# Kernel optimization log

Measured on AMD Instinct MI355X. Metric: run time of the kernel, lower is better.

## Reference

```python
import jax, jax.numpy as jnp
import numpy as np

H = 4          # heads (both HGTConv and MHA)
LN_EPS = 1e-5
ALPHA = 0.1


def _ln(x, g, b):
    m = x.mean(-1, keepdims=True)
    v = ((x - m) ** 2).mean(-1, keepdims=True)
    return (x - m) * jax.lax.rsqrt(v + LN_EPS) * g + b


def _kqv(x, Wk, bk, Wq, bq, Wv, bv, D):
    N = x.shape[0]
    k = (x @ Wk.T + bk).reshape(N, H, D)
    q = (x @ Wq.T + bq).reshape(N, H, D)
    v = (x @ Wv.T + bv).reshape(N, H, D)
    return k, q, v


def _hgt_edge(q_dst, k_src, v_src, a_rel, m_rel, p_rel, src, dst, n_dst):
    """PyG HGTConv message passing for one edge type: relation-transform,
    per-dst-node softmax, weighted scatter-sum."""
    D = q_dst.shape[-1]
    k = jnp.einsum('nhd,hde->nhe', k_src, a_rel)   # [N_src,H,D]
    v = jnp.einsum('nhd,hde->nhe', v_src, m_rel)
    logit = (q_dst[dst] * k[src]).sum(-1) * p_rel / np.sqrt(D)   # [E,H]
    mx = jax.ops.segment_max(logit, dst, num_segments=n_dst)
    e = jnp.exp(logit - mx[dst])
    s = jax.ops.segment_sum(e, dst, num_segments=n_dst)
    a = e / (s[dst] + 1e-16)
    return jax.ops.segment_sum(v[src] * a[..., None], dst, num_segments=n_dst)  # [N_dst,H,D]


def _hgt_out(agg, x, Wout, bout, skip):
    N, dim = x.shape
    o = jax.nn.gelu(agg.reshape(N, dim), approximate=False) @ Wout.T + bout
    a = jax.nn.sigmoid(skip)
    return a * o + (1.0 - a) * x


def _mha(x, Wi, bi, Wo, bo):
    # self-attention over all entities as a single sequence (batch=1)
    N, dim = x.shape
    D = dim // H
    q, k, v = jnp.split(x @ Wi.T + bi, 3, axis=-1)
    q = q.reshape(N, H, D).transpose(1, 0, 2)
    k = k.reshape(N, H, D).transpose(1, 0, 2)
    v = v.reshape(N, H, D).transpose(1, 0, 2)
    att = jax.nn.softmax(jnp.einsum('hnd,hmd->hnm', q, k) / np.sqrt(D), axis=-1)
    o = jnp.einsum('hnm,hmd->hnd', att, v).transpose(1, 0, 2).reshape(N, dim)
    return o @ Wo.T + bo


def _forward(x_entity, x_passage, query_emb,
             Wk_ent, bk_ent, Wq_ent, bq_ent, Wv_ent, bv_ent, Wout_ent, bout_ent, skip_ent,
             Wk_psg, bk_psg, Wq_psg, bq_psg, Wv_psg, bv_psg, Wout_psg, bout_psg, skip_psg,
             a_e2p, m_e2p, p_e2p, a_p2e, m_p2e, p_p2e,
             mha_in_w, mha_in_b, mha_out_w, mha_out_b,
             ln_ent_g, ln_ent_b, ln_psg_g, ln_psg_b,
             w1, b1, w2, b2,
             e2p_src, e2p_dst, p2e_src, p2e_dst):
    N_e, dim = x_entity.shape
    N_p = x_passage.shape[0]
    D = dim // H
    # ---- HGTConv ----
    k_e, q_e, v_e = _kqv(x_entity, Wk_ent, bk_ent, Wq_ent, bq_ent, Wv_ent, bv_ent, D)
    k_p, q_p, v_p = _kqv(x_passage, Wk_psg, bk_psg, Wq_psg, bq_psg, Wv_psg, bv_psg, D)
    agg_p = _hgt_edge(q_p, k_e, v_e, a_e2p, m_e2p, p_e2p, e2p_src, e2p_dst, N_p)
    agg_e = _hgt_edge(q_e, k_p, v_p, a_p2e, m_p2e, p_p2e, p2e_src, p2e_dst, N_e)
    h_ent = _hgt_out(agg_e, x_entity, Wout_ent, bout_ent, skip_ent)
    h_psg = _hgt_out(agg_p, x_passage, Wout_psg, bout_psg, skip_psg)
    # ---- global entity attention + residual mix + LN ----
    h_glob = _mha(h_ent, mha_in_w, mha_in_b, mha_out_w, mha_out_b)
    h_ent = _ln((1.0 - ALPHA) * h_ent + ALPHA * h_glob, ln_ent_g, ln_ent_b)
    # ---- gather-scale-scatter entity -> passage (kernel target) ----
    q = query_emb.reshape(-1)
    rel = jax.nn.sigmoid(h_ent @ q)                          # [N_e]
    w_ent = h_ent[e2p_src] * rel[e2p_src][:, None]           # gather + scale
    ctx = jax.ops.segment_sum(w_ent, e2p_dst, num_segments=N_p)  # scatter-add
    h_psg = _ln(h_psg + ctx, ln_psg_g, ln_psg_b)
    # ---- scoring head ----
    feats = jnp.concatenate([h_psg, jnp.broadcast_to(q, (N_p, dim))], axis=-1)
    scores = (jax.nn.relu(feats @ w1.T + b1) @ w2.T + b2).squeeze(-1)
    return scores


def setup_inputs() -> dict:
    key = jax.random.key(0)
    N_E, N_P, DIM, NE = 4096, 4096, 256, 262144
    D = DIM // H
    ks = iter(jax.random.split(key, 64))
    def rn(shape, s=1.0):
        return jax.random.normal(next(ks), shape, jnp.float32) * s
    w = 0.05
    inp = {
        'x_entity': rn((N_E, DIM)),
        'x_passage': rn((N_P, DIM)),
        'query_emb': rn((DIM,)),
    }
    for t in ('ent', 'psg'):
        inp['Wk_' + t] = rn((DIM, DIM), w); inp['bk_' + t] = jnp.zeros((DIM,))
        inp['Wq_' + t] = rn((DIM, DIM), w); inp['bq_' + t] = jnp.zeros((DIM,))
        inp['Wv_' + t] = rn((DIM, DIM), w); inp['bv_' + t] = jnp.zeros((DIM,))
        inp['Wout_' + t] = rn((DIM, DIM), w); inp['bout_' + t] = jnp.zeros((DIM,))
        inp['skip_' + t] = jnp.ones(())
    for e in ('e2p', 'p2e'):
        inp['a_' + e] = rn((H, D, D), w)
        inp['m_' + e] = rn((H, D, D), w)
        inp['p_' + e] = jnp.ones((H,))
    inp['mha_in_w'] = rn((3 * DIM, DIM), w); inp['mha_in_b'] = jnp.zeros((3 * DIM,))
    inp['mha_out_w'] = rn((DIM, DIM), w); inp['mha_out_b'] = jnp.zeros((DIM,))
    inp['ln_ent_g'] = jnp.ones((DIM,)); inp['ln_ent_b'] = jnp.zeros((DIM,))
    inp['ln_psg_g'] = jnp.ones((DIM,)); inp['ln_psg_b'] = jnp.zeros((DIM,))
    inp['w1'] = rn((DIM, 2 * DIM), w); inp['b1'] = jnp.zeros((DIM,))
    inp['w2'] = rn((1, DIM), w); inp['b2'] = jnp.zeros((1,))
    inp['e2p_src'] = jax.random.randint(next(ks), (NE,), 0, N_E, jnp.int32)
    inp['e2p_dst'] = jax.random.randint(next(ks), (NE,), 0, N_P, jnp.int32)
    inp['p2e_src'] = jax.random.randint(next(ks), (NE,), 0, N_P, jnp.int32)
    inp['p2e_dst'] = jax.random.randint(next(ks), (NE,), 0, N_E, jnp.int32)
    return inp


def reference(x_entity, x_passage, query_emb,
              Wk_ent, bk_ent, Wq_ent, bq_ent, Wv_ent, bv_ent, Wout_ent, bout_ent, skip_ent,
              Wk_psg, bk_psg, Wq_psg, bq_psg, Wv_psg, bv_psg, Wout_psg, bout_psg, skip_psg,
              a_e2p, m_e2p, p_e2p, a_p2e, m_p2e, p_p2e,
              mha_in_w, mha_in_b, mha_out_w, mha_out_b,
              ln_ent_g, ln_ent_b, ln_psg_g, ln_psg_b,
              w1, b1, w2, b2,
              e2p_src, e2p_dst, p2e_src, p2e_dst):
    return _forward(x_entity, x_passage, query_emb,
                    Wk_ent, bk_ent, Wq_ent, bq_ent, Wv_ent, bv_ent, Wout_ent, bout_ent, skip_ent,
                    Wk_psg, bk_psg, Wq_psg, bq_psg, Wv_psg, bv_psg, Wout_psg, bout_psg, skip_psg,
                    a_e2p, m_e2p, p_e2p, a_p2e, m_p2e, p_p2e,
                    mha_in_w, mha_in_b, mha_out_w, mha_out_b,
                    ln_ent_g, ln_ent_b, ln_psg_g, ln_psg_b,
                    w1, b1, w2, b2,
                    e2p_src, e2p_dst, p2e_src, p2e_dst)
```

## Files before the change

### kernel.cpp

```cpp
#include <hip/hip_runtime.h>
#include <hip/hip_bf16.h>
#include <math.h>

#define DIM 256
#define NHEAD 4
#define HD 64
#define MSPLIT 4

typedef __attribute__((ext_vector_type(8))) short short8b;
typedef __attribute__((ext_vector_type(4))) float f32x4;

union B8 { uint4 u; short8b v; };

__device__ __forceinline__ float sigmoidf_(float x) { return 1.0f / (1.0f + __expf(-x)); }
__device__ __forceinline__ float geluf_(float x) {
    return 0.5f * x * (1.0f + erff(x * 0.70710678118654752440f));
}
__device__ __forceinline__ float wave_sum64(float v) {
    v += __shfl_xor(v, 32); v += __shfl_xor(v, 16); v += __shfl_xor(v, 8);
    v += __shfl_xor(v, 4);  v += __shfl_xor(v, 2);  v += __shfl_xor(v, 1);
    return v;
}
__device__ __forceinline__ unsigned short f2bf(float f) {
    union { float f; unsigned int u; } a; a.f = f;
    unsigned int u = a.u;
    unsigned int r = (u + 0x7FFFu + ((u >> 16) & 1u)) >> 16;
    return (unsigned short)r;
}
__device__ __forceinline__ unsigned int pk2bf(float lo, float hi) {
    return (unsigned int)f2bf(lo) | ((unsigned int)f2bf(hi) << 16);
}

template<int DO_GELU>
__launch_bounds__(256)
__global__ void cvt_bf16_kernel(const float* __restrict__ src,
                                unsigned short* __restrict__ dst, int n8)
{
    const int i = blockIdx.x * 256 + threadIdx.x;
    if (i >= n8) return;
    float4 a = reinterpret_cast<const float4*>(src)[2 * i];
    float4 b = reinterpret_cast<const float4*>(src)[2 * i + 1];
    if (DO_GELU) {
        a.x = geluf_(a.x); a.y = geluf_(a.y); a.z = geluf_(a.z); a.w = geluf_(a.w);
        b.x = geluf_(b.x); b.y = geluf_(b.y); b.z = geluf_(b.z); b.w = geluf_(b.w);
    }
    ushort4 lo = {f2bf(a.x), f2bf(a.y), f2bf(a.z), f2bf(a.w)};
    ushort4 hi = {f2bf(b.x), f2bf(b.y), f2bf(b.z), f2bf(b.w)};
    reinterpret_cast<ushort4*>(dst)[2 * i] = lo;
    reinterpret_cast<ushort4*>(dst)[2 * i + 1] = hi;
}

__launch_bounds__(256)
__global__ void cvt_w_kernel(const float* __restrict__ W0, const float* __restrict__ W1,
                             const float* __restrict__ W2, const float* __restrict__ W3,
                             const float* __restrict__ W4, const float* __restrict__ W5,
                             const float* __restrict__ W6, const float* __restrict__ W7,
                             const float* __restrict__ W8, const float* __restrict__ W9,
                             const float* __restrict__ W10, const float* __restrict__ W11,
                             unsigned short* __restrict__ arena)
{
    const float* s;
    switch (blockIdx.y) {
        case 0: s = W0; break;  case 1: s = W1; break;  case 2: s = W2; break;
        case 3: s = W3; break;  case 4: s = W4; break;  case 5: s = W5; break;
        case 6: s = W6; break;  case 7: s = W7; break;  case 8: s = W8; break;
        case 9: s = W9; break;  case 10: s = W10; break; default: s = W11; break;
    }
    const int i = blockIdx.x * 256 + threadIdx.x;
    unsigned short* dst = arena + (size_t)blockIdx.y * 65536;
    float4 a = reinterpret_cast<const float4*>(s)[2 * i];
    float4 b = reinterpret_cast<const float4*>(s)[2 * i + 1];
    ushort4 lo = {f2bf(a.x), f2bf(a.y), f2bf(a.z), f2bf(a.w)};
    ushort4 hi = {f2bf(b.x), f2bf(b.y), f2bf(b.z), f2bf(b.w)};
    reinterpret_cast<ushort4*>(dst)[2 * i] = lo;
    reinterpret_cast<ushort4*>(dst)[2 * i + 1] = hi;
}

template<int OUT_MODE, int WF32, int WBF>
__launch_bounds__(256)
__global__ void bgemm_kernel(const unsigned short* __restrict__ Abf,
                             const unsigned short* __restrict__ W0b,
                             const unsigned short* __restrict__ W1b,
                             const unsigned short* __restrict__ W2b,
                             const float* __restrict__ B0, const float* __restrict__ B1,
                             const float* __restrict__ B2,
                             float* __restrict__ C, int ldc,
                             unsigned short* __restrict__ Cbf, int ldcb,
                             const float* __restrict__ xres,
                             const float* __restrict__ skipv)
{
    const int t = threadIdx.x;
    const int lane = t & 63;
    const int wid = t >> 6;
    const int col16 = lane & 15;
    const int oct = lane >> 4;
    const int r0 = blockIdx.y * 64 + wid * 16;
    const int c0 = blockIdx.x * 64;
    const int widx = c0 >> 8;
    const unsigned short* W = (widx == 0) ? W0b : (widx == 1 ? W1b : W2b);
    const float* Bv = (widx == 0) ? B0 : (widx == 1 ? B1 : B2);
    const int cw = c0 & 255;

    const unsigned short* aptr = Abf + (size_t)(r0 + col16) * 256 + oct * 8;
    const unsigned short* wptr = W + (size_t)(cw + col16) * 256 + oct * 8;

    f32x4 acc0 = {0,0,0,0}, acc1 = {0,0,0,0}, acc2 = {0,0,0,0}, acc3 = {0,0,0,0};
#pragma unroll
    for (int k0 = 0; k0 < 256; k0 += 32) {
        B8 af, w0, w1, w2, w3;
        af.u = *reinterpret_cast<const uint4*>(aptr + k0);
        w0.u = *reinterpret_cast<const uint4*>(wptr + k0);
        w1.u = *reinterpret_cast<const uint4*>(wptr + k0 + 16 * 256);
        w2.u = *reinterpret_cast<const uint4*>(wptr + k0 + 32 * 256);
        w3.u = *reinterpret_cast<const uint4*>(wptr + k0 + 48 * 256);
        acc0 = __builtin_amdgcn_mfma_f32_16x16x32_bf16(af.v, w0.v, acc0, 0, 0, 0);
        acc1 = __builtin_amdgcn_mfma_f32_16x16x32_bf16(af.v, w1.v, acc1, 0, 0, 0);
        acc2 = __builtin_amdgcn_mfma_f32_16x16x32_bf16(af.v, w2.v, acc2, 0, 0, 0);
        acc3 = __builtin_amdgcn_mfma_f32_16x16x32_bf16(af.v, w3.v, acc3, 0, 0, 0);
    }

    float bias[4];
#pragma unroll
    for (int j = 0; j < 4; ++j) bias[j] = Bv[cw + j * 16 + col16];
    float sg = 0.f;
    if (OUT_MODE == 1) sg = sigmoidf_(skipv[0]);

    const float av[4][4] = {
        {acc0.x, acc0.y, acc0.z, acc0.w}, {acc1.x, acc1.y, acc1.z, acc1.w},
        {acc2.x, acc2.y, acc2.z, acc2.w}, {acc3.x, acc3.y, acc3.z, acc3.w}};
#pragma unroll
    for (int r = 0; r < 4; ++r) {
        const int row = r0 + oct * 4 + r;
#pragma unroll
        for (int j = 0; j < 4; ++j) {
            const int col = c0 + j * 16 + col16;
            float v = av[j][r] + bias[j];
            if (OUT_MODE == 1) {
                const float xv = xres[(size_t)row * ldc + col];
                v = sg * v + (1.f - sg) * xv;
            }
            if (WF32) C[(size_t)row * ldc + col] = v;
            if (WBF)  Cbf[(size_t)row * ldcb + col] = f2bf(v);
        }
    }
}

template<int IN_GELU, int OUT_MODE>
__launch_bounds__(256)
__global__ void gemm_kernel(const float* __restrict__ A, int lda,
                            const float* __restrict__ W0, const float* __restrict__ W1,
                            const float* __restrict__ W2, int ldw,
                            const float* __restrict__ B0, const float* __restrict__ B1,
                            const float* __restrict__ B2,
                            float* __restrict__ C, int ldc, int Kin,
                            float* __restrict__ scores,
                            const float* __restrict__ w2v,
                            const float* __restrict__ b2v)
{
    __shared__ float As[16][68];
    __shared__ float Ws[16][68];
    const int t = threadIdx.x;
    const int r0 = blockIdx.y * 64;
    const int c0 = blockIdx.x * 64;
    const int widx = c0 >> 8;
    const float* W  = (widx == 0) ? W0 : (widx == 1 ? W1 : W2);
    const float* Bv = (widx == 0) ? B0 : (widx == 1 ? B1 : B2);
    const int cw = c0 & 255;

    const int lrow = t >> 2;
    const int lk   = (t & 3) << 2;
    const int ty = t >> 4, tx = t & 15;

    const float* Aptr = A + (size_t)(r0 + lrow) * lda + lk;
    const float* Wptr = W + (size_t)(cw + lrow) * ldw + lk;

    float acc[4][4] = {};
    for (int k0 = 0; k0 < Kin; k0 += 16) {
        float4 av = *reinterpret_cast<const float4*>(Aptr + k0);
        float4 wv = *reinterpret_cast<const float4*>(Wptr + k0);
        if (IN_GELU) {
            av.x = geluf_(av.x); av.y = geluf_(av.y);
            av.z = geluf_(av.z); av.w = geluf_(av.w);
        }
        As[lk + 0][lrow] = av.x; As[lk + 1][lrow] = av.y;
        As[lk + 2][lrow] = av.z; As[lk + 3][lrow] = av.w;
        Ws[lk + 0][lrow] = wv.x; Ws[lk + 1][lrow] = wv.y;
        Ws[lk + 2][lrow] = wv.z; Ws[lk + 3][lrow] = wv.w;
        __syncthreads();
#pragma unroll
        for (int k = 0; k < 16; ++k) {
            const float4 a = *reinterpret_cast<const float4*>(&As[k][ty << 2]);
            const float4 b = *reinterpret_cast<const float4*>(&Ws[k][tx << 2]);
            const float ar[4] = {a.x, a.y, a.z, a.w};
            const float br[4] = {b.x, b.y, b.z, b.w};
#pragma unroll
            for (int i = 0; i < 4; ++i)
#pragma unroll
                for (int j = 0; j < 4; ++j)
                    acc[i][j] = fmaf(ar[i], br[j], acc[i][j]);
        }
        __syncthreads();
    }

    float bias[4];
#pragma unroll
    for (int j = 0; j < 4; ++j) bias[j] = Bv[cw + (tx << 2) + j];

    if (OUT_MODE == 0) {
#pragma unroll
        for (int i = 0; i < 4; ++i) {
            float4 st;
            st.x = acc[i][0] + bias[0]; st.y = acc[i][1] + bias[1];
            st.z = acc[i][2] + bias[2]; st.w = acc[i][3] + bias[3];
            *reinterpret_cast<float4*>(&C[(size_t)(r0 + (ty << 2) + i) * ldc + c0 + (tx << 2)]) = st;
        }
    } else {
        float wv[4];
#pragma unroll
        for (int j = 0; j < 4; ++j) wv[j] = w2v[c0 + (tx << 2) + j];
#pragma unroll
        for (int i = 0; i < 4; ++i) {
            float p = 0.f;
#pragma unroll
            for (int j = 0; j < 4; ++j)
                p = fmaf(fmaxf(acc[i][j] + bias[j], 0.f), wv[j], p);
            if (c0 == 0 && tx == 0) p += b2v[0];
            atomicAdd(&scores[r0 + (ty << 2) + i], p);
        }
    }
}

__launch_bounds__(256)
__global__ void rel_transform_kernel(const float* __restrict__ kin, int ldin,
                                     const float* __restrict__ arel,
                                     float* __restrict__ kout)
{
    __shared__ float Al[64][68];
    __shared__ float Kl[64][65];
    const int t = threadIdx.x;
    const int r0 = blockIdx.x * 64;
    const int h = blockIdx.y;
    const float* ah = arel + h * 4096;
    for (int i = t; i < 1024; i += 256) {
        const int rr = i >> 4, c4 = (i & 15) << 2;
        const float4 av = *reinterpret_cast<const float4*>(&ah[rr * 64 + c4]);
        *reinterpret_cast<float4*>(&Al[rr][c4]) = av;
        const float4 kv = *reinterpret_cast<const float4*>(&kin[(size_t)(r0 + rr) * ldin + h * 64 + c4]);
        Kl[rr][c4 + 0] = kv.x; Kl[rr][c4 + 1] = kv.y;
        Kl[rr][c4 + 2] = kv.z; Kl[rr][c4 + 3] = kv.w;
    }
    __syncthreads();
    const int r  = t & 63;
    const int e0 = (t >> 6) << 4;
    float acc[16] = {};
    for (int d = 0; d < 64; ++d) {
        const float kv = Kl[r][d];
#pragma unroll
        for (int u4 = 0; u4 < 4; ++u4) {
            const float4 a = *reinterpret_cast<const float4*>(&Al[d][e0 + (u4 << 2)]);
            acc[u4 * 4 + 0] = fmaf(kv, a.x, acc[u4 * 4 + 0]);
            acc[u4 * 4 + 1] = fmaf(kv, a.y, acc[u4 * 4 + 1]);
            acc[u4 * 4 + 2] = fmaf(kv, a.z, acc[u4 * 4 + 2]);
            acc[u4 * 4 + 3] = fmaf(kv, a.w, acc[u4 * 4 + 3]);
        }
    }
#pragma unroll
    for (int u4 = 0; u4 < 4; ++u4) {
        float4 st = {acc[u4 * 4 + 0], acc[u4 * 4 + 1], acc[u4 * 4 + 2], acc[u4 * 4 + 3]};
        *reinterpret_cast<float4*>(&kout[(size_t)(r0 + r) * 256 + h * 64 + e0 + (u4 << 2)]) = st;
    }
}

__global__ void edge_count_kernel(const int* __restrict__ dst, int* __restrict__ cnt, int E)
{
    const int i = blockIdx.x * 256 + threadIdx.x;
    if (i < E) atomicAdd(&cnt[dst[i]], 1);
}

__launch_bounds__(1024)
__global__ void scan_kernel(const int* __restrict__ cnt, int* __restrict__ indptr,
                            int* __restrict__ cursor)
{
    __shared__ int sh[1024];
    const int t = threadIdx.x;
    const int4 v = *reinterpret_cast<const int4*>(&cnt[t << 2]);
    const int sum = v.x + v.y + v.z + v.w;
    sh[t] = sum;
    __syncthreads();
    for (int off = 1; off < 1024; off <<= 1) {
        int x = 0;
        if (t >= off) x = sh[t - off];
        __syncthreads();
        if (t >= off) sh[t] += x;
        __syncthreads();
    }
    int run = sh[t] - sum;
    const int base = t << 2;
    if (t == 0) indptr[0] = 0;
    cursor[base + 0] = run; run += v.x; indptr[base + 1] = run;
    cursor[base + 1] = run; run += v.y; indptr[base + 2] = run;
    cursor[base + 2] = run; run += v.z; indptr[base + 3] = run;
    cursor[base + 3] = run; run += v.w; indptr[base + 4] = run;
}

__global__ void edge_scatter_kernel(const int* __restrict__ src, const int* __restrict__ dst,
                                    int* __restrict__ cursor, int* __restrict__ ssrc, int E)
{
    const int i = blockIdx.x * 256 + threadIdx.x;
    if (i < E) {
        const int p = atomicAdd(&cursor[dst[i]], 1);
        ssrc[p] = src[i];
    }
}

__launch_bounds__(256)
__global__ void hgt_attn_kernel(const float* __restrict__ qdst,
                                const float* __restrict__ kt,
                                const float* __restrict__ vt,
                                const float* __restrict__ prel,
                                const int* __restrict__ indptr,
                                const int* __restrict__ ssrc,
                                float* __restrict__ agg)
{
    const int n = blockIdx.x * 4 + (threadIdx.x >> 6);
    const int lane = threadIdx.x & 63;
    const int h = lane >> 4;
    const int d4 = (lane & 15) << 2;
    const float4 q = *reinterpret_cast<const float4*>(&qdst[(size_t)n * 768 + h * 64 + d4]);
    const float ps = prel[h] * 0.125f;
    const int e0 = indptr[n], e1 = indptr[n + 1];
    float m = -1e30f, s = 0.f;
    float4 acc = {0.f, 0.f, 0.f, 0.f};
    for (int e = e0; e < e1; ++e) {
        const int sr = ssrc[e];
        const float4 k = *reinterpret_cast<const float4*>(&kt[(size_t)sr * 256 + h * 64 + d4]);
        float d = q.x * k.x + q.y * k.y + q.z * k.z + q.w * k.w;
        d += __shfl_xor(d, 1); d += __shfl_xor(d, 2);
        d += __shfl_xor(d, 4); d += __shfl_xor(d, 8);
        const float logit = d * ps;
        const float mn = fmaxf(m, logit);
        const float f = __expf(m - mn);
        const float p = __expf(logit - mn);
        s = s * f + p;
        const float4 v = *reinterpret_cast<const float4*>(&vt[(size_t)sr * 256 + h * 64 + d4]);
        acc.x = acc.x * f + p * v.x;
        acc.y = acc.y * f + p * v.y;
        acc.z = acc.z * f + p * v.z;
        acc.w = acc.w * f + p * v.w;
        m = mn;
    }
    const float inv = 1.f / (s + 1e-16f);
    float4 st = {acc.x * inv, acc.y * inv, acc.z * inv, acc.w * inv};
    *reinterpret_cast<float4*>(&agg[(size_t)n * 256 + h * 64 + d4]) = st;
}

__launch_bounds__(256)
__global__ void vtrans_kernel(const unsigned short* __restrict__ qkv_bf,
                              unsigned short* __restrict__ vt, int N)
{
    __shared__ unsigned short tile[64][66];
    const int t = threadIdx.x;
    const int k0 = blockIdx.x * 64;
    const int h = blockIdx.y;
    {
        const int key = t >> 2;
        const int d0 = (t & 3) << 4;
        const unsigned short* src = qkv_bf + (size_t)(k0 + key) * 768 + 512 + h * 64 + d0;
        const uint4 a = *reinterpret_cast<const uint4*>(src);
        const uint4 b = *reinterpret_cast<const uint4*>(src + 8);
        const unsigned int w_[8] = {a.x, a.y, a.z, a.w, b.x, b.y, b.z, b.w};
#pragma unroll
        for (int j = 0; j < 8; ++j) {
            tile[d0 + 2 * j][key]     = (unsigned short)(w_[j] & 0xffff);
            tile[d0 + 2 * j + 1][key] = (unsigned short)(w_[j] >> 16);
        }
    }
    __syncthreads();
    {
        const int d = t >> 2;
        const int kk = (t & 3) << 4;
        unsigned int o_[8];
#pragma unroll
        for (int j = 0; j < 8; ++j)
            o_[j] = (unsigned int)tile[d][kk + 2 * j] | ((unsigned int)tile[d][kk + 2 * j + 1] << 16);
        unsigned short* dstp = vt + (size_t)(h * 64 + d) * N + k0 + kk;
        uint4 s0 = {o_[0], o_[1], o_[2], o_[3]};
        uint4 s1 = {o_[4], o_[5], o_[6], o_[7]};
        *reinterpret_cast<uint4*>(dstp) = s0;
        *reinterpret_cast<uint4*>(dstp + 8) = s1;
    }
}

__launch_bounds__(256)
__global__ void mha_mfma_kernel(const unsigned short* __restrict__ qkv_bf,
                                const unsigned short* __restrict__ vt_bf,
                                float* __restrict__ opart,
                                float* __restrict__ mpart,
                                float* __restrict__ lpart,
                                int N)
{
    const int lane = threadIdx.x & 63;
    const int g = lane >> 4;
    const int q15 = lane & 15;
    const int gw = blockIdx.x * 4 + (threadIdx.x >> 6);
    const int split = gw & (MSPLIT - 1);
    const int gq = gw >> 2;
    const int h = gq >> 8;
    const int qt = gq & 255;
    const int q0 = qt * 16;
    const int kbeg = split * (N / MSPLIT);
    const int kend = kbeg + (N / MSPLIT);

    B8 qf0, qf1;
    {
        const unsigned short* qp = qkv_bf + (size_t)(q0 + q15) * 768 + h * 64 + g * 8;
        qf0.u = *reinterpret_cast<const uint4*>(qp);
        qf1.u = *reinterpret_cast<const uint4*>(qp + 32);
    }

    f32x4 o0 = {0,0,0,0}, o1 = {0,0,0,0}, o2 = {0,0,0,0}, o3 = {0,0,0,0};
    float m_run = -1e30f, l_run = 0.f;

    const unsigned short* kbase = qkv_bf + 256 + h * 64 + g * 8;
    const unsigned short* vbase = vt_bf + (size_t)(h * 64 + q15) * N + g * 8;
    const int sl0 = (((2 * g) & 3) << 4) + q15;
    const int sl1 = (((2 * g + 1) & 3) << 4) + q15;

    for (int ck = kbeg; ck < kend; ck += 32) {
        B8 k00, k01, k10, k11;
        const unsigned short* kp0 = kbase + (size_t)(ck + q15) * 768;
        const unsigned short* kp1 = kbase + (size_t)(ck + 16 + q15) * 768;
        k00.u = *reinterpret_cast<const uint4*>(kp0);
        k01.u = *reinterpret_cast<const uint4*>(kp0 + 32);
        k10.u = *reinterpret_cast<const uint4*>(kp1);
        k11.u = *reinterpret_cast<const uint4*>(kp1 + 32);
        f32x4 s0 = {0,0,0,0}, s1 = {0,0,0,0};
        s0 = __builtin_amdgcn_mfma_f32_16x16x32_bf16(k00.v, qf0.v, s0, 0, 0, 0);
        s0 = __builtin_amdgcn_mfma_f32_16x16x32_bf16(k01.v, qf1.v, s0, 0, 0, 0);
        s1 = __builtin_amdgcn_mfma_f32_16x16x32_bf16(k10.v, qf0.v, s1, 0, 0, 0);
        s1 = __builtin_amdgcn_mfma_f32_16x16x32_bf16(k11.v, qf1.v, s1, 0, 0, 0);

        float p[8];
        p[0] = s0.x * 0.125f; p[1] = s0.y * 0.125f; p[2] = s0.z * 0.125f; p[3] = s0.w * 0.125f;
        p[4] = s1.x * 0.125f; p[5] = s1.y * 0.125f; p[6] = s1.z * 0.125f; p[7] = s1.w * 0.125f;

        float mx = fmaxf(fmaxf(fmaxf(p[0], p[1]), fmaxf(p[2], p[3])),
                         fmaxf(fmaxf(p[4], p[5]), fmaxf(p[6], p[7])));
        mx = fmaxf(mx, __shfl_xor(mx, 16));
        mx = fmaxf(mx, __shfl_xor(mx, 32));
        const float mnew = fmaxf(m_run, mx);
        const float f = __expf(m_run - mnew);
        float sum = 0.f;
#pragma unroll
        for (int i = 0; i < 8; ++i) { p[i] = __expf(p[i] - mnew); sum += p[i]; }
        sum += __shfl_xor(sum, 16);
        sum += __shfl_xor(sum, 32);
        l_run = l_run * f + sum;
        m_run = mnew;
        o0 *= f; o1 *= f; o2 *= f; o3 *= f;

        const unsigned int c01a = pk2bf(p[0], p[1]), c23a = pk2bf(p[2], p[3]);
        const unsigned int c01b = pk2bf(p[4], p[5]), c23b = pk2bf(p[6], p[7]);
        uint4 pu;
        {
            unsigned int x0, x1;
            x0 = (unsigned int)__shfl((int)c01a, sl0); x1 = (unsigned int)__shfl((int)c01b, sl0);
            pu.x = (g < 2) ? x0 : x1;
            x0 = (unsigned int)__shfl((int)c23a, sl0); x1 = (unsigned int)__shfl((int)c23b, sl0);
            pu.y = (g < 2) ? x0 : x1;
            x0 = (unsigned int)__shfl((int)c01a, sl1); x1 = (unsigned int)__shfl((int)c01b, sl1);
            pu.z = (g < 2) ? x0 : x1;
            x0 = (unsigned int)__shfl((int)c23a, sl1); x1 = (unsigned int)__shfl((int)c23b, sl1);
            pu.w = (g < 2) ? x0 : x1;
        }
        B8 pb; pb.u = pu;

        const unsigned short* vp = vbase + ck;
        B8 vf;
        vf.u = *reinterpret_cast<const uint4*>(vp);
        o0 = __builtin_amdgcn_mfma_f32_16x16x32_bf16(vf.v, pb.v, o0, 0, 0, 0);
        vf.u = *reinterpret_cast<const uint4*>(vp + (size_t)16 * N);
        o1 = __builtin_amdgcn_mfma_f32_16x16x32_bf16(vf.v, pb.v, o1, 0, 0, 0);
        vf.u = *reinterpret_cast<const uint4*>(vp + (size_t)32 * N);
        o2 = __builtin_amdgcn_mfma_f32_16x16x32_bf16(vf.v, pb.v, o2, 0, 0, 0);
        vf.u = *reinterpret_cast<const uint4*>(vp + (size_t)48 * N);
        o3 = __builtin_amdgcn_mfma_f32_16x16x32_bf16(vf.v, pb.v, o3, 0, 0, 0);
    }

    float* op = opart + (size_t)split * N * 256 + (size_t)(q0 + q15) * 256 + h * 64 + 4 * g;
#pragma unroll
    for (int r = 0; r < 4; ++r) {
        op[0 * 16 + r] = o0[r];
        op[1 * 16 + r] = o1[r];
        op[2 * 16 + r] = o2[r];
        op[3 * 16 + r] = o3[r];
    }
    if (g == 0) {
        mpart[(size_t)(split * NHEAD + h) * N + q0 + q15] = m_run;
        lpart[(size_t)(split * NHEAD + h) * N + q0 + q15] = l_run;
    }
}

__launch_bounds__(256)
__global__ void mha_combine_kernel(const float* __restrict__ opart,
                                   const float* __restrict__ mpart,
                                   const float* __restrict__ lpart,
                                   unsigned short* __restrict__ outpb, int N)
{
    const int q = blockIdx.x;
    const int c = threadIdx.x;
    const int h = c >> 6;
    const size_t base = (size_t)q * 256 + c;
    float m[MSPLIT], l[MSPLIT];
    float M = -1e30f;
#pragma unroll
    for (int s = 0; s < MSPLIT; ++s) {
        m[s] = mpart[(size_t)(s * NHEAD + h) * N + q];
        l[s] = lpart[(size_t)(s * NHEAD + h) * N + q];
        M = fmaxf(M, m[s]);
    }
    float L = 0.f, o = 0.f;
#pragma unroll
    for (int s = 0; s < MSPLIT; ++s) {
        const float w = __expf(m[s] - M);
        L += w * l[s];
        o = fmaf(w, opart[(size_t)s * N * 256 + base], o);
    }
    outpb[base] = f2bf(o / L);
}

__launch_bounds__(256)
__global__ void mix_ln_rel_kernel(float* __restrict__ he, const float* __restrict__ hg,
                                  const float* __restrict__ g, const float* __restrict__ b,
                                  const float* __restrict__ q, float* __restrict__ rel)
{
    const int row = (blockIdx.x * 256 + threadIdx.x) >> 6;
    const int lane = threadIdx.x & 63;
    const float4 a = *reinterpret_cast<const float4*>(&he[(size_t)row * 256 + (lane << 2)]);
    const float4 c = *reinterpret_cast<const float4*>(&hg[(size_t)row * 256 + (lane << 2)]);
    float4 v;
    v.x = 0.9f * a.x + 0.1f * c.x; v.y = 0.9f * a.y + 0.1f * c.y;
    v.z = 0.9f * a.z + 0.1f * c.z; v.w = 0.9f * a.w + 0.1f * c.w;
    const float mean = wave_sum64(v.x + v.y + v.z + v.w) * (1.f / 256.f);
    float4 d = {v.x - mean, v.y - mean, v.z - mean, v.w - mean};
    const float var = wave_sum64(d.x * d.x + d.y * d.y + d.z * d.z + d.w * d.w) * (1.f / 256.f);
    const float rs = rsqrtf(var + 1e-5f);
    const float4 gg = *reinterpret_cast<const float4*>(&g[lane << 2]);
    const float4 bb = *reinterpret_cast<const float4*>(&b[lane << 2]);
    float4 y = {d.x * rs * gg.x + bb.x, d.y * rs * gg.y + bb.y,
                d.z * rs * gg.z + bb.z, d.w * rs * gg.w + bb.w};
    *reinterpret_cast<float4*>(&he[(size_t)row * 256 + (lane << 2)]) = y;
    const float4 qq = *reinterpret_cast<const float4*>(&q[lane << 2]);
    const float dq = wave_sum64(y.x * qq.x + y.y * qq.y + y.z * qq.z + y.w * qq.w);
    if (lane == 0) rel[row] = sigmoidf_(dq);
}

__launch_bounds__(256)
__global__ void ctx_gather_kernel(const float* __restrict__ he, const float* __restrict__ rel,
                                  const int* __restrict__ indptr, const int* __restrict__ ssrc,
                                  float* __restrict__ ctx)
{
    const int gw = (blockIdx.x * 256 + threadIdx.x) >> 6;
    const int lane = threadIdx.x & 63;
    const int p = gw >> 2, qt = gw & 3;
    const int e0 = indptr[p], e1 = indptr[p + 1];
    float acc = 0.f;
    for (int e = e0; e < e1; ++e) {
        const int sr = ssrc[e];
        acc = fmaf(he[(size_t)sr * 256 + qt * 64 + lane], rel[sr], acc);
    }
    ctx[(size_t)p * 256 + qt * 64 + lane] = acc;
}

__launch_bounds__(256)
__global__ void psg_ln_kernel(float* __restrict__ hp, const float* __restrict__ ctx,
                              const float* __restrict__ g, const float* __restrict__ b)
{
    const int row = (blockIdx.x * 256 + threadIdx.x) >> 6;
    const int lane = threadIdx.x & 63;
    const float4 a = *reinterpret_cast<const float4*>(&hp[(size_t)row * 256 + (lane << 2)]);
    const float4 c = *reinterpret_cast<const float4*>(&ctx[(size_t)row * 256 + (lane << 2)]);
    float4 v = {a.x + c.x, a.y + c.y, a.z + c.z, a.w + c.w};
    const float mean = wave_sum64(v.x + v.y + v.z + v.w) * (1.f / 256.f);
    float4 d = {v.x - mean, v.y - mean, v.z - mean, v.w - mean};
    const float var = wave_sum64(d.x * d.x + d.y * d.y + d.z * d.z + d.w * d.w) * (1.f / 256.f);
    const float rs = rsqrtf(var + 1e-5f);
    const float4 gg = *reinterpret_cast<const float4*>(&g[lane << 2]);
    const float4 bb = *reinterpret_cast<const float4*>(&b[lane << 2]);
    float4 y = {d.x * rs * gg.x + bb.x, d.y * rs * gg.y + bb.y,
                d.z * rs * gg.z + bb.z, d.w * rs * gg.w + bb.w};
    *reinterpret_cast<float4*>(&hp[(size_t)row * 256 + (lane << 2)]) = y;
}

__global__ void qterm_kernel(const float* __restrict__ w1, const float* __restrict__ b1,
                             const float* __restrict__ q, float* __restrict__ qterm)
{
    __shared__ float qs[256];
    const int t = threadIdx.x;
    qs[t] = q[t];
    __syncthreads();
    float s = b1[t];
    for (int k = 0; k < 256; ++k) s = fmaf(w1[(size_t)t * 512 + 256 + k], qs[k], s);
    qterm[t] = s;
}

extern "C" void kernel_launch(void* const* d_in, const int* in_sizes, int n_in,
                              void* d_out, int out_size, void* d_ws, size_t ws_size,
                              hipStream_t stream)
{
    const float* x_ent = (const float*)d_in[0];
    const float* x_psg = (const float*)d_in[1];
    const float* q_emb = (const float*)d_in[2];
    const float* Wk_e = (const float*)d_in[3];  const float* bk_e = (const float*)d_in[4];
    const float* Wq_e = (const float*)d_in[5];  const float* bq_e = (const float*)d_in[6];
    const float* Wv_e = (const float*)d_in[7];  const float* bv_e = (const float*)d_in[8];
    const float* Wo_e = (const float*)d_in[9];  const float* bo_e = (const float*)d_in[10];
    const float* sk_e = (const float*)d_in[11];
    const float* Wk_p = (const float*)d_in[12]; const float* bk_p = (const float*)d_in[13];
    const float* Wq_p = (const float*)d_in[14]; const float* bq_p = (const float*)d_in[15];
    const float* Wv_p = (const float*)d_in[16]; const float* bv_p = (const float*)d_in[17];
    const float* Wo_p = (const float*)d_in[18]; const float* bo_p = (const float*)d_in[19];
    const float* sk_p = (const float*)d_in[20];
    const float* a_e2p = (const float*)d_in[21];
    const float* m_e2p = (const float*)d_in[22];
    const float* p_e2p = (const float*)d_in[23];
    const float* a_p2e = (const float*)d_in[24];
    const float* m_p2e = (const float*)d_in[25];
    const float* p_p2e = (const float*)d_in[26];
    const float* Wmi = (const float*)d_in[27];  const float* bmi = (const float*)d_in[28];
    const float* Wmo = (const float*)d_in[29];  const float* bmo = (const float*)d_in[30];
    const float* lng_e = (const float*)d_in[31]; const float* lnb_e = (const float*)d_in[32];
    const float* lng_p = (const float*)d_in[33]; const float* lnb_p = (const float*)d_in[34];
    const float* w1 = (const float*)d_in[35];   const float* b1 = (const float*)d_in[36];
    const float* w2 = (const float*)d_in[37];   const float* b2 = (const float*)d_in[38];
    const int* e2p_src = (const int*)d_in[39];
    const int* e2p_dst = (const int*)d_in[40];
    const int* p2e_src = (const int*)d_in[41];
    const int* p2e_dst = (const int*)d_in[42];

    const int NE = in_sizes[0] / DIM;
    const int NP = in_sizes[1] / DIM;
    const int E  = in_sizes[39];
    float* scores = (float*)d_out;

    char* wp = (char*)d_ws;
    auto alloc = [&](size_t bytes) -> void* {
        void* r = (void*)wp;
        wp += (bytes + 255) & ~(size_t)255;
        return r;
    };
    float* kqv_e = (float*)alloc((size_t)NE * 768 * 4);
    float* kqv_p = (float*)alloc((size_t)NP * 768 * 4);
    float* kt_e  = (float*)alloc((size_t)NE * 256 * 4);
    float* vt_e  = (float*)alloc((size_t)NE * 256 * 4);
    float* kt_p  = (float*)alloc((size_t)NP * 256 * 4);
    float* vt_p  = (float*)alloc((size_t)NP * 256 * 4);
    float* agg_p = (float*)alloc((size_t)NP * 256 * 4);
    float* agg_e = (float*)alloc((size_t)NE * 256 * 4);
    float* h_ent = (float*)alloc((size_t)NE * 256 * 4);
    float* h_psg = (float*)alloc((size_t)NP * 256 * 4);
    float* h_glob= (float*)alloc((size_t)NE * 256 * 4);
    float* relv  = (float*)alloc((size_t)NE * 4);
    float* ctxb  = (float*)alloc((size_t)NP * 256 * 4);
    float* qterm = (float*)alloc(256 * 4);
    unsigned short* warena  = (unsigned short*)alloc((size_t)12 * 65536 * 2);
    unsigned short* xe_bf   = (unsigned short*)alloc((size_t)NE * 256 * 2);
    unsigned short* xp_bf   = (unsigned short*)alloc((size_t)NP * 256 * 2);
    unsigned short* ge_bf   = (unsigned short*)alloc((size_t)NE * 256 * 2);
    unsigned short* gp_bf   = (unsigned short*)alloc((size_t)NP * 256 * 2);
    unsigned short* hent_bf = (unsigned short*)alloc((size_t)NE * 256 * 2);
    unsigned short* atto_bf = (unsigned short*)alloc((size_t)NE * 256 * 2);
    unsigned short* qkv_bf  = (unsigned short*)alloc((size_t)NE * 768 * 2);
    unsigned short* vt_bf   = (unsigned short*)alloc((size_t)256 * NE * 2);
    float* mpart = (float*)alloc((size_t)MSPLIT * NHEAD * NE * 4);
    float* lpart = (float*)alloc((size_t)MSPLIT * NHEAD * NE * 4);
    float* opart = kqv_e;
    int* cnt_a = (int*)alloc((size_t)NP * 4);
    int* cur_a = (int*)alloc((size_t)NP * 4);
    int* ip_a  = (int*)alloc((size_t)(NP + 1) * 4);
    int* ss_a  = (int*)alloc((size_t)E * 4);
    int* cnt_b = (int*)alloc((size_t)NE * 4);
    int* cur_b = (int*)alloc((size_t)NE * 4);
    int* ip_b  = (int*)alloc((size_t)(NE + 1) * 4);
    int* ss_b  = (int*)alloc((size_t)E * 4);

    hipMemsetAsync(cnt_a, 0, (size_t)NP * 4, stream);
    hipMemsetAsync(cnt_b, 0, (size_t)NE * 4, stream);
    hipMemsetAsync(d_out, 0, (size_t)out_size * 4, stream);

    cvt_w_kernel<<<dim3(32, 12), 256, 0, stream>>>(
        Wk_e, Wq_e, Wv_e, Wo_e, Wk_p, Wq_p, Wv_p, Wo_p,
        Wmi, Wmi + 65536, Wmi + 131072, Wmo, warena);
    cvt_bf16_kernel<0><<<NE * 256 / 2048, 256, 0, stream>>>(x_ent, xe_bf, NE * 32);
    cvt_bf16_kernel<0><<<NP * 256 / 2048, 256, 0, stream>>>(x_psg, xp_bf, NP * 32);

    const int eb = (E + 255) / 256;
    edge_count_kernel<<<eb, 256, 0, stream>>>(e2p_dst, cnt_a, E);
    edge_count_kernel<<<eb, 256, 0, stream>>>(p2e_dst, cnt_b, E);
    scan_kernel<<<1, 1024, 0, stream>>>(cnt_a, ip_a, cur_a);
    scan_kernel<<<1, 1024, 0, stream>>>(cnt_b, ip_b, cur_b);
    edge_scatter_kernel<<<eb, 256, 0, stream>>>(e2p_src, e2p_dst, cur_a, ss_a, E);
    edge_scatter_kernel<<<eb, 256, 0, stream>>>(p2e_src, p2e_dst, cur_b, ss_b, E);

    bgemm_kernel<0,1,0><<<dim3(12, NE / 64), 256, 0, stream>>>(
        xe_bf, warena, warena + 65536, warena + 131072, bk_e, bq_e, bv_e,
        kqv_e, 768, nullptr, 0, nullptr, nullptr);
    bgemm_kernel<0,1,0><<<dim3(12, NP / 64), 256, 0, stream>>>(
        xp_bf, warena + 4*65536, warena + 5*65536, warena + 6*65536, bk_p, bq_p, bv_p,
        kqv_p, 768, nullptr, 0, nullptr, nullptr);

    rel_transform_kernel<<<dim3(NE / 64, NHEAD), 256, 0, stream>>>(kqv_e + 0,   768, a_e2p, kt_e);
    rel_transform_kernel<<<dim3(NE / 64, NHEAD), 256, 0, stream>>>(kqv_e + 512, 768, m_e2p, vt_e);
    rel_transform_kernel<<<dim3(NP / 64, NHEAD), 256, 0, stream>>>(kqv_p + 0,   768, a_p2e, kt_p);
    rel_transform_kernel<<<dim3(NP / 64, NHEAD), 256, 0, stream>>>(kqv_p + 512, 768, m_p2e, vt_p);

    hgt_attn_kernel<<<NP / 4, 256, 0, stream>>>(kqv_p + 256, kt_e, vt_e, p_e2p, ip_a, ss_a, agg_p);
    hgt_attn_kernel<<<NE / 4, 256, 0, stream>>>(kqv_e + 256, kt_p, vt_p, p_p2e, ip_b, ss_b, agg_e);

    cvt_bf16_kernel<1><<<NE * 256 / 2048, 256, 0, stream>>>(agg_e, ge_bf, NE * 32);
    cvt_bf16_kernel<1><<<NP * 256 / 2048, 256, 0, stream>>>(agg_p, gp_bf, NP * 32);
    bgemm_kernel<1,1,1><<<dim3(4, NE / 64), 256, 0, stream>>>(
        ge_bf, warena + 3*65536, warena + 3*65536, warena + 3*65536, bo_e, bo_e, bo_e,
        h_ent, 256, hent_bf, 256, x_ent, sk_e);
    bgemm_kernel<1,1,0><<<dim3(4, NP / 64), 256, 0, stream>>>(
        gp_bf, warena + 7*65536, warena + 7*65536, warena + 7*65536, bo_p, bo_p, bo_p,
        h_psg, 256, nullptr, 0, x_psg, sk_p);

    bgemm_kernel<0,0,1><<<dim3(12, NE / 64), 256, 0, stream>>>(
        hent_bf, warena + 8*65536, warena + 9*65536, warena + 10*65536,
        bmi, bmi + 256, bmi + 512,
        nullptr, 0, qkv_bf, 768, nullptr, nullptr);
    vtrans_kernel<<<dim3(NE / 64, NHEAD), 256, 0, stream>>>(qkv_bf, vt_bf, NE);
    mha_mfma_kernel<<<NHEAD * (NE / 16) * MSPLIT / 4, 256, 0, stream>>>(
        qkv_bf, vt_bf, opart, mpart, lpart, NE);
    mha_combine_kernel<<<NE, 256, 0, stream>>>(opart, mpart, lpart, atto_bf, NE);
    bgemm_kernel<0,1,0><<<dim3(4, NE / 64), 256, 0, stream>>>(
        atto_bf, warena + 11*65536, warena + 11*65536, warena + 11*65536, bmo, bmo, bmo,
        h_glob, 256, nullptr, 0, nullptr, nullptr);

    mix_ln_rel_kernel<<<NE / 4, 256, 0, stream>>>(h_ent, h_glob, lng_e, lnb_e, q_emb, relv);

    ctx_gather_kernel<<<NP, 256, 0, stream>>>(h_ent, relv, ip_a, ss_a, ctxb);
    psg_ln_kernel<<<NP / 4, 256, 0, stream>>>(h_psg, ctxb, lng_p, lnb_p);

    qterm_kernel<<<1, 256, 0, stream>>>(w1, b1, q_emb, qterm);
    gemm_kernel<0,2><<<dim3(4, NP / 64), 256, 0, stream>>>(
        h_psg, 256, w1, w1, w1, 512, qterm, qterm, qterm,
        nullptr, 256, 256, scores, w2, b2);
}
```

Measured before the change: 717.2 us.

## Rewrite MHA kernel with 32x32 MFMA tiles, permlane swaps, and prefetch HGT gathers

The flash-attention style MHA kernel now uses 32x32x16 bf16 MFMA on 32-query tiles instead of 16x16x32 on 16-query tiles. It builds the P operand with the hardware packed bf16 convert and permlane32 swaps rather than many shuffles, and doubles the key split count to keep enough waves in flight. The HGT edge attention loop also software-prefetches the next edge's K/V rows. This aims to cut cross-lane shuffle overhead and memory latency stalls, at the cost of higher register pressure and larger partial buffers for the combine step.

```diff
diff --git a/kernel.cpp b/kernel.cpp
--- a/kernel.cpp
+++ b/kernel.cpp
@@ -5,10 +5,12 @@
 #define DIM 256
 #define NHEAD 4
 #define HD 64
-#define MSPLIT 4
+#define MSPLIT 8
 
 typedef __attribute__((ext_vector_type(8))) short short8b;
 typedef __attribute__((ext_vector_type(4))) float f32x4;
+typedef __attribute__((ext_vector_type(16))) float f32x16;
+typedef __attribute__((ext_vector_type(2))) unsigned int uint2v;
 
 union B8 { uint4 u; short8b v; };
 
@@ -27,8 +29,13 @@
     unsigned int r = (u + 0x7FFFu + ((u >> 16) & 1u)) >> 16;
     return (unsigned short)r;
 }
-__device__ __forceinline__ unsigned int pk2bf(float lo, float hi) {
-    return (unsigned int)f2bf(lo) | ((unsigned int)f2bf(hi) << 16);
+__device__ __forceinline__ unsigned int cvtpk_(float lo, float hi) {
+    unsigned int r;
+    asm("v_cvt_pk_bf16_f32 %0, %1, %2" : "=v"(r) : "v"(lo), "v"(hi));
+    return r;
+}
+__device__ __forceinline__ uint2v plswap_(unsigned int a, unsigned int b) {
+    return __builtin_amdgcn_permlane32_swap(a, b, false, false);
 }
 
 template<int DO_GELU>
@@ -331,9 +338,17 @@
     const int e0 = indptr[n], e1 = indptr[n + 1];
     float m = -1e30f, s = 0.f;
     float4 acc = {0.f, 0.f, 0.f, 0.f};
+    float4 kc = {0.f, 0.f, 0.f, 0.f}, vc = {0.f, 0.f, 0.f, 0.f};
+    if (e0 < e1) {
+        const int sr0 = ssrc[e0];
+        kc = *reinterpret_cast<const float4*>(&kt[(size_t)sr0 * 256 + h * 64 + d4]);
+        vc = *reinterpret_cast<const float4*>(&vt[(size_t)sr0 * 256 + h * 64 + d4]);
+    }
     for (int e = e0; e < e1; ++e) {
-        const int sr = ssrc[e];
-        const float4 k = *reinterpret_cast<const float4*>(&kt[(size_t)sr * 256 + h * 64 + d4]);
+        const float4 k = kc, v = vc;
+        const int nsr = ssrc[(e + 1 < e1) ? (e + 1) : e];
+        kc = *reinterpret_cast<const float4*>(&kt[(size_t)nsr * 256 + h * 64 + d4]);
+        vc = *reinterpret_cast<const float4*>(&vt[(size_t)nsr * 256 + h * 64 + d4]);
         float d = q.x * k.x + q.y * k.y + q.z * k.z + q.w * k.w;
         d += __shfl_xor(d, 1); d += __shfl_xor(d, 2);
         d += __shfl_xor(d, 4); d += __shfl_xor(d, 8);
@@ -342,7 +357,6 @@
         const float f = __expf(m - mn);
         const float p = __expf(logit - mn);
         s = s * f + p;
-        const float4 v = *reinterpret_cast<const float4*>(&vt[(size_t)sr * 256 + h * 64 + d4]);
         acc.x = acc.x * f + p * v.x;
         acc.y = acc.y * f + p * v.y;
         acc.z = acc.z * f + p * v.z;
@@ -400,104 +414,113 @@
                                 int N)
 {
     const int lane = threadIdx.x & 63;
-    const int g = lane >> 4;
-    const int q15 = lane & 15;
+    const int l31 = lane & 31;
+    const int hi = lane >> 5;
     const int gw = blockIdx.x * 4 + (threadIdx.x >> 6);
     const int split = gw & (MSPLIT - 1);
-    const int gq = gw >> 2;
-    const int h = gq >> 8;
-    const int qt = gq & 255;
-    const int q0 = qt * 16;
+    const int gq = gw / MSPLIT;
+    const int h = gq >> 7;
+    const int qt = gq & 127;
+    const int q0 = qt * 32;
     const int kbeg = split * (N / MSPLIT);
     const int kend = kbeg + (N / MSPLIT);
 
-    B8 qf0, qf1;
+    B8 qf0, qf1, qf2, qf3;
     {
-        const unsigned short* qp = qkv_bf + (size_t)(q0 + q15) * 768 + h * 64 + g * 8;
+        const unsigned short* qp = qkv_bf + (size_t)(q0 + l31) * 768 + h * 64 + hi * 8;
         qf0.u = *reinterpret_cast<const uint4*>(qp);
-        qf1.u = *reinterpret_cast<const uint4*>(qp + 32);
-    }
-
-    f32x4 o0 = {0,0,0,0}, o1 = {0,0,0,0}, o2 = {0,0,0,0}, o3 = {0,0,0,0};
+        qf1.u = *reinterpret_cast<const uint4*>(qp + 16);
+        qf2.u = *reinterpret_cast<const uint4*>(qp + 32);
+        qf3.u = *reinterpret_cast<const uint4*>(qp + 48);
+    }
+
+    f32x16 o0, o1;
+#pragma unroll
+    for (int i = 0; i < 16; ++i) { o0[i] = 0.f; o1[i] = 0.f; }
     float m_run = -1e30f, l_run = 0.f;
 
-    const unsigned short* kbase = qkv_bf + 256 + h * 64 + g * 8;
-    const unsigned short* vbase = vt_bf + (size_t)(h * 64 + q15) * N + g * 8;
-    const int sl0 = (((2 * g) & 3) << 4) + q15;
-    const int sl1 = (((2 * g + 1) & 3) << 4) + q15;
+    const unsigned short* kbase = qkv_bf + 256 + h * 64 + hi * 8;
+    const unsigned short* vbase = vt_bf + (size_t)(h * 64 + l31) * N + hi * 8;
 
     for (int ck = kbeg; ck < kend; ck += 32) {
-        B8 k00, k01, k10, k11;
-        const unsigned short* kp0 = kbase + (size_t)(ck + q15) * 768;
-        const unsigned short* kp1 = kbase + (size_t)(ck + 16 + q15) * 768;
-        k00.u = *reinterpret_cast<const uint4*>(kp0);
-        k01.u = *reinterpret_cast<const uint4*>(kp0 + 32);
-        k10.u = *reinterpret_cast<const uint4*>(kp1);
-        k11.u = *reinterpret_cast<const uint4*>(kp1 + 32);
-        f32x4 s0 = {0,0,0,0}, s1 = {0,0,0,0};
-        s0 = __builtin_amdgcn_mfma_f32_16x16x32_bf16(k00.v, qf0.v, s0, 0, 0, 0);
-        s0 = __builtin_amdgcn_mfma_f32_16x16x32_bf16(k01.v, qf1.v, s0, 0, 0, 0);
-        s1 = __builtin_amdgcn_mfma_f32_16x16x32_bf16(k10.v, qf0.v, s1, 0, 0, 0);
-        s1 = __builtin_amdgcn_mfma_f32_16x16x32_bf16(k11.v, qf1.v, s1, 0, 0, 0);
-
-        float p[8];
-        p[0] = s0.x * 0.125f; p[1] = s0.y * 0.125f; p[2] = s0.z * 0.125f; p[3] = s0.w * 0.125f;
-        p[4] = s1.x * 0.125f; p[5] = s1.y * 0.125f; p[6] = s1.z * 0.125f; p[7] = s1.w * 0.125f;
-
-        float mx = fmaxf(fmaxf(fmaxf(p[0], p[1]), fmaxf(p[2], p[3])),
-                         fmaxf(fmaxf(p[4], p[5]), fmaxf(p[6], p[7])));
-        mx = fmaxf(mx, __shfl_xor(mx, 16));
-        mx = fmaxf(mx, __shfl_xor(mx, 32));
+        const unsigned short* kp = kbase + (size_t)(ck + l31) * 768;
+        B8 kf0, kf1, kf2, kf3;
+        kf0.u = *reinterpret_cast<const uint4*>(kp);
+        kf1.u = *reinterpret_cast<const uint4*>(kp + 16);
+        kf2.u = *reinterpret_cast<const uint4*>(kp + 32);
+        kf3.u = *reinterpret_cast<const uint4*>(kp + 48);
+        const unsigned short* vp = vbase + ck;
+        B8 vf00, vf01, vf10, vf11;
+        vf00.u = *reinterpret_cast<const uint4*>(vp);
+        vf01.u = *reinterpret_cast<const uint4*>(vp + 16);
+        vf10.u = *reinterpret_cast<const uint4*>(vp + (size_t)32 * N);
+        vf11.u = *reinterpret_cast<const uint4*>(vp + (size_t)32 * N + 16);
+
+        f32x16 s;
+#pragma unroll
+        for (int i = 0; i < 16; ++i) s[i] = 0.f;
+        s = __builtin_amdgcn_mfma_f32_32x32x16_bf16(kf0.v, qf0.v, s, 0, 0, 0);
+        s = __builtin_amdgcn_mfma_f32_32x32x16_bf16(kf1.v, qf1.v, s, 0, 0, 0);
+        s = __builtin_amdgcn_mfma_f32_32x32x16_bf16(kf2.v, qf2.v, s, 0, 0, 0);
+        s = __builtin_amdgcn_mfma_f32_32x32x16_bf16(kf3.v, qf3.v, s, 0, 0, 0);
+
+        float mx = s[0];
+#pragma unroll
+        for (int i = 1; i < 16; ++i) mx = fmaxf(mx, s[i]);
+        mx *= 0.125f;
+        {
+            uint2v mr = plswap_(__float_as_uint(mx), __float_as_uint(mx));
+            mx = fmaxf(__uint_as_float(mr[0]), __uint_as_float(mr[1]));
+        }
         const float mnew = fmaxf(m_run, mx);
         const float f = __expf(m_run - mnew);
+        m_run = mnew;
+
+        float p[16];
         float sum = 0.f;
 #pragma unroll
-        for (int i = 0; i < 8; ++i) { p[i] = __expf(p[i] - mnew); sum += p[i]; }
-        sum += __shfl_xor(sum, 16);
-        sum += __shfl_xor(sum, 32);
+        for (int i = 0; i < 16; ++i) {
+            p[i] = __expf(fmaf(s[i], 0.125f, -mnew));
+            sum += p[i];
+        }
         l_run = l_run * f + sum;
-        m_run = mnew;
-        o0 *= f; o1 *= f; o2 *= f; o3 *= f;
-
-        const unsigned int c01a = pk2bf(p[0], p[1]), c23a = pk2bf(p[2], p[3]);
-        const unsigned int c01b = pk2bf(p[4], p[5]), c23b = pk2bf(p[6], p[7]);
-        uint4 pu;
-        {
-            unsigned int x0, x1;
-            x0 = (unsigned int)__shfl((int)c01a, sl0); x1 = (unsigned int)__shfl((int)c01b, sl0);
-            pu.x = (g < 2) ? x0 : x1;
-            x0 = (unsigned int)__shfl((int)c23a, sl0); x1 = (unsigned int)__shfl((int)c23b, sl0);
-            pu.y = (g < 2) ? x0 : x1;
-            x0 = (unsigned int)__shfl((int)c01a, sl1); x1 = (unsigned int)__shfl((int)c01b, sl1);
-            pu.z = (g < 2) ? x0 : x1;
-            x0 = (unsigned int)__shfl((int)c23a, sl1); x1 = (unsigned int)__shfl((int)c23b, sl1);
-            pu.w = (g < 2) ? x0 : x1;
-        }
-        B8 pb; pb.u = pu;
-
-        const unsigned short* vp = vbase + ck;
-        B8 vf;
-        vf.u = *reinterpret_cast<const uint4*>(vp);
-        o0 = __builtin_amdgcn_mfma_f32_16x16x32_bf16(vf.v, pb.v, o0, 0, 0, 0);
-        vf.u = *reinterpret_cast<const uint4*>(vp + (size_t)16 * N);
-        o1 = __builtin_amdgcn_mfma_f32_16x16x32_bf16(vf.v, pb.v, o1, 0, 0, 0);
-        vf.u = *reinterpret_cast<const uint4*>(vp + (size_t)32 * N);
-        o2 = __builtin_amdgcn_mfma_f32_16x16x32_bf16(vf.v, pb.v, o2, 0, 0, 0);
-        vf.u = *reinterpret_cast<const uint4*>(vp + (size_t)48 * N);
-        o3 = __builtin_amdgcn_mfma_f32_16x16x32_bf16(vf.v, pb.v, o3, 0, 0, 0);
-    }
-
-    float* op = opart + (size_t)split * N * 256 + (size_t)(q0 + q15) * 256 + h * 64 + 4 * g;
-#pragma unroll
-    for (int r = 0; r < 4; ++r) {
-        op[0 * 16 + r] = o0[r];
-        op[1 * 16 + r] = o1[r];
-        op[2 * 16 + r] = o2[r];
-        op[3 * 16 + r] = o3[r];
-    }
-    if (g == 0) {
-        mpart[(size_t)(split * NHEAD + h) * N + q0 + q15] = m_run;
-        lpart[(size_t)(split * NHEAD + h) * N + q0 + q15] = l_run;
+        o0 *= f;
+        o1 *= f;
+
+        unsigned int w0 = cvtpk_(p[0], p[1]),  w1 = cvtpk_(p[2], p[3]);
+        unsigned int w2 = cvtpk_(p[4], p[5]),  w3 = cvtpk_(p[6], p[7]);
+        unsigned int w4 = cvtpk_(p[8], p[9]),  w5 = cvtpk_(p[10], p[11]);
+        unsigned int w6 = cvtpk_(p[12], p[13]), w7 = cvtpk_(p[14], p[15]);
+        uint2v r02 = plswap_(w0, w2);
+        uint2v r13 = plswap_(w1, w3);
+        uint2v r46 = plswap_(w4, w6);
+        uint2v r57 = plswap_(w5, w7);
+        B8 pb0, pb1;
+        pb0.u = (uint4){r02[0], r13[0], r02[1], r13[1]};
+        pb1.u = (uint4){r46[0], r57[0], r46[1], r57[1]};
+
+        o0 = __builtin_amdgcn_mfma_f32_32x32x16_bf16(vf00.v, pb0.v, o0, 0, 0, 0);
+        o0 = __builtin_amdgcn_mfma_f32_32x32x16_bf16(vf01.v, pb1.v, o0, 0, 0, 0);
+        o1 = __builtin_amdgcn_mfma_f32_32x32x16_bf16(vf10.v, pb0.v, o1, 0, 0, 0);
+        o1 = __builtin_amdgcn_mfma_f32_32x32x16_bf16(vf11.v, pb1.v, o1, 0, 0, 0);
+    }
+
+    {
+        uint2v lr = plswap_(__float_as_uint(l_run), __float_as_uint(l_run));
+        l_run = __uint_as_float(lr[0]) + __uint_as_float(lr[1]);
+    }
+
+    float* op = opart + ((size_t)split * N + q0 + l31) * 256 + h * 64 + 4 * hi;
+#pragma unroll
+    for (int u = 0; u < 4; ++u) {
+        float4 s0_ = {o0[4 * u + 0], o0[4 * u + 1], o0[4 * u + 2], o0[4 * u + 3]};
+        *reinterpret_cast<float4*>(op + 8 * u) = s0_;
+        float4 s1_ = {o1[4 * u + 0], o1[4 * u + 1], o1[4 * u + 2], o1[4 * u + 3]};
+        *reinterpret_cast<float4*>(op + 32 + 8 * u) = s1_;
+    }
+    if (hi == 0) {
+        mpart[((size_t)split * NHEAD + h) * N + q0 + l31] = m_run;
+        lpart[((size_t)split * NHEAD + h) * N + q0 + l31] = l_run;
     }
 }
 
@@ -731,7 +754,7 @@
         bmi, bmi + 256, bmi + 512,
         nullptr, 0, qkv_bf, 768, nullptr, nullptr);
     vtrans_kernel<<<dim3(NE / 64, NHEAD), 256, 0, stream>>>(qkv_bf, vt_bf, NE);
-    mha_mfma_kernel<<<NHEAD * (NE / 16) * MSPLIT / 4, 256, 0, stream>>>(
+    mha_mfma_kernel<<<NHEAD * (NE / 32) * MSPLIT / 4, 256, 0, stream>>>(
         qkv_bf, vt_bf, opart, mpart, lpart, NE);
     mha_combine_kernel<<<NE, 256, 0, stream>>>(opart, mpart, lpart, atto_bf, NE);
     bgemm_kernel<0,1,0><<<dim3(4, NE / 64), 256, 0, stream>>>(
```

New measurement: 673.7 us. 6.1% less time.
